# Performance work log

Hardware: AMD Instinct MI355X
Metric: run time of the kernel (lower is better)

The kernel has to match this reference:

```python
import jax, jax.numpy as jnp
import numpy as np

VOCAB = 50257
EMB = 256
HID = 512
BATCH = 32
SEQ = 512
PAD_ID = 0


def setup_inputs() -> dict:
    key = jax.random.key(0)
    k1, k2, k3, k4, k5, k6 = jax.random.split(key, 6)
    input_ids = jax.random.randint(k1, (BATCH, SEQ), 0, VOCAB, dtype=jnp.int32)
    attention_mask = jax.random.randint(k2, (BATCH, SEQ), 0, 2, dtype=jnp.int32)
    # learned params
    embed_table = jax.random.normal(k3, (VOCAB, EMB), dtype=jnp.float32) * 0.02
    Wx = jax.random.normal(k4, (EMB, HID), dtype=jnp.float32) / np.sqrt(EMB)
    Wh = jax.random.normal(k5, (HID, HID), dtype=jnp.float32) / np.sqrt(HID)
    b = jnp.zeros((HID,), dtype=jnp.float32)
    return {"input_ids": input_ids, "attention_mask": attention_mask,
            "embed_table": embed_table, "Wx": Wx, "Wh": Wh, "b": b}


def reference(input_ids, attention_mask, embed_table, Wx, Wh, b):
    # Embedding lookup: [B, S, E]
    emb = embed_table[input_ids]
    # time-major for scan: [S, B, E] and [S, B]
    xs = jnp.swapaxes(emb, 0, 1)
    ms = jnp.swapaxes(attention_mask, 0, 1)
    h0 = jnp.zeros((emb.shape[0], Wh.shape[0]), dtype=emb.dtype)

    def step(h, xm):
        x_t, m_t = xm  # [B, E], [B]
        h_new = jnp.tanh(x_t @ Wx + h @ Wh + b)  # Elman RNN cell
        h_next = jnp.where((m_t != PAD_ID)[:, None], h_new, h)
        return h_next, h_next

    final_h, all_h_tmajor = jax.lax.scan(step, h0, (xs, ms))
    all_h = jnp.swapaxes(all_h_tmajor, 0, 1)  # [B, S, H]
    return all_h, final_h
```

## Files before the change

kernel.cpp:

```cpp
#include <hip/hip_runtime.h>

#define VOCAB 50257
#define EMB 256
#define HID 512
#define BATCH 32
#define SEQ 512

typedef _Float16 h2 __attribute__((ext_vector_type(2)));

#if __has_builtin(__builtin_amdgcn_fdot2)
#define FDOT2(a, b, c) __builtin_amdgcn_fdot2((a), (b), (c), false)
#else
static __device__ __forceinline__ float FDOT2(h2 a, h2 b, float c) {
    return c + (float)a.x * (float)b.x + (float)a.y * (float)b.y;
}
#endif

static __device__ __forceinline__ h2 mk2(float a, float b) {
    h2 r; r.x = (_Float16)a; r.y = (_Float16)b; return r;
}

__global__ __launch_bounds__(256) void xprec_kernel(
    const int* __restrict__ ids, const float* __restrict__ emb,
    const float* __restrict__ Wx, const float* __restrict__ bias,
    float* __restrict__ allh)
{
    __shared__ float embL[16][EMB];
    const int tid  = threadIdx.x;
    const int tok0 = blockIdx.x * 16;

    {
        const int t    = tid >> 4;
        const int part = tid & 15;
        const int id   = ids[tok0 + t];
        const float4* src = (const float4*)(emb + (size_t)id * EMB + part * 16);
        float4* dst = (float4*)(&embL[t][part * 16]);
        dst[0] = src[0]; dst[1] = src[1]; dst[2] = src[2]; dst[3] = src[3];
    }
    __syncthreads();

    const int j0 = tid * 2;
    float2 acc[16];
    const float2 bv = *(const float2*)(bias + j0);
#pragma unroll
    for (int t = 0; t < 16; ++t) acc[t] = bv;

    for (int e = 0; e < EMB; e += 4) {
        const float2 w0 = *(const float2*)(Wx + (size_t)(e + 0) * HID + j0);
        const float2 w1 = *(const float2*)(Wx + (size_t)(e + 1) * HID + j0);
        const float2 w2 = *(const float2*)(Wx + (size_t)(e + 2) * HID + j0);
        const float2 w3 = *(const float2*)(Wx + (size_t)(e + 3) * HID + j0);
#pragma unroll
        for (int t = 0; t < 16; ++t) {
            const float4 ev = *(const float4*)(&embL[t][e]);
            acc[t].x += ev.x * w0.x + ev.y * w1.x + ev.z * w2.x + ev.w * w3.x;
            acc[t].y += ev.x * w0.y + ev.y * w1.y + ev.z * w2.y + ev.w * w3.y;
        }
    }

#pragma unroll
    for (int t = 0; t < 16; ++t) {
        *(float2*)(allh + (size_t)(tok0 + t) * HID + j0) = acc[t];
    }
}

__global__ __launch_bounds__(512, 2) void rnn_local_kernel(
    const int* __restrict__ mask, const float* __restrict__ Wh,
    float* __restrict__ allh, float* __restrict__ finalh)
{
    __shared__ h2    wlds[2][32][512];
    __shared__ float zp[8][8][64];
    __shared__ h2    h2L[256];
    __shared__ int   mlist[SEQ];
    __shared__ int   nmL;

    const int tid = threadIdx.x;
    const int b   = blockIdx.x;
    const int c   = tid & 63;
    const int p   = tid >> 6;

    int* maskL = (int*)zp;
    maskL[tid] = mask[b * SEQ + tid];
    __syncthreads();
    if (tid == 0) {
        int n = 0;
        for (int t = 0; t < SEQ; ++t) if (maskL[t]) mlist[n++] = t;
        nmL = n;
    }

    const float* wb = Wh + (size_t)(64 * p) * HID + c;
    h2 wv0[32], wv1[32], wv2[32], wv3[32], wv4[32], wv5[32];
#pragma unroll
    for (int i = 0; i < 32; ++i) {
        const float* r0 = wb + (size_t)(2 * i) * HID;
        const float* r1 = r0 + HID;
        wv0[i] = mk2(r0[0 * 64], r1[0 * 64]);
        wv1[i] = mk2(r0[1 * 64], r1[1 * 64]);
        wv2[i] = mk2(r0[2 * 64], r1[2 * 64]);
        wv3[i] = mk2(r0[3 * 64], r1[3 * 64]);
        wv4[i] = mk2(r0[4 * 64], r1[4 * 64]);
        wv5[i] = mk2(r0[5 * 64], r1[5 * 64]);
        wlds[0][i][tid] = mk2(r0[6 * 64], r1[6 * 64]);
        wlds[1][i][tid] = mk2(r0[7 * 64], r1[7 * 64]);
    }
    if (tid < 256) h2L[tid] = mk2(0.f, 0.f);

    __syncthreads();
    const int nm = nmL;

    float* arow = allh + (size_t)b * SEQ * HID;

    {
        const int end0 = nm ? mlist[0] : SEQ;
        for (int t = 0; t < end0; ++t) arow[(size_t)t * HID + tid] = 0.f;
    }

    float hreg  = 0.f;
    float xnext = 0.f;
    if (nm) xnext = arow[(size_t)mlist[0] * HID + tid];

    for (int i = 0; i < nm; ++i) {
        const int t    = mlist[i];
        const int tend = (i + 1 < nm) ? mlist[i + 1] : SEQ;
        const float x  = xnext;
        if (i + 1 < nm)
            xnext = arow[(size_t)mlist[i + 1] * HID + tid];

        float a0 = 0.f, a1 = 0.f, a2 = 0.f, a3 = 0.f;
        float a4 = 0.f, a5 = 0.f, a6 = 0.f, a7 = 0.f;
        const h2* hp = &h2L[32 * p];
#pragma unroll
        for (int i2 = 0; i2 < 32; ++i2) {
            const h2 hv = hp[i2];
            a0 = FDOT2(wv0[i2], hv, a0);
            a1 = FDOT2(wv1[i2], hv, a1);
            a2 = FDOT2(wv2[i2], hv, a2);
            a3 = FDOT2(wv3[i2], hv, a3);
            a4 = FDOT2(wv4[i2], hv, a4);
            a5 = FDOT2(wv5[i2], hv, a5);
            a6 = FDOT2(wlds[0][i2][tid], hv, a6);
            a7 = FDOT2(wlds[1][i2][tid], hv, a7);
        }
        zp[p][0][c] = a0; zp[p][1][c] = a1; zp[p][2][c] = a2; zp[p][3][c] = a3;
        zp[p][4][c] = a4; zp[p][5][c] = a5; zp[p][6][c] = a6; zp[p][7][c] = a7;
        __syncthreads();

        const float z = zp[0][p][c] + zp[1][p][c] + zp[2][p][c] + zp[3][p][c]
                      + zp[4][p][c] + zp[5][p][c] + zp[6][p][c] + zp[7][p][c];
        const float hn = tanhf(x + z);
        hreg = hn;
        ((_Float16*)h2L)[tid] = (_Float16)hn;
        for (int tt = t; tt < tend; ++tt)
            arow[(size_t)tt * HID + tid] = hreg;
        __syncthreads();
    }
    finalh[b * HID + tid] = hreg;
}

extern "C" void kernel_launch(void* const* d_in, const int* in_sizes, int n_in,
                              void* d_out, int out_size, void* d_ws, size_t ws_size,
                              hipStream_t stream) {
    const int*   ids  = (const int*)d_in[0];
    const int*   msk  = (const int*)d_in[1];
    const float* emb  = (const float*)d_in[2];
    const float* Wx   = (const float*)d_in[3];
    const float* Wh   = (const float*)d_in[4];
    const float* bias = (const float*)d_in[5];

    float* allh   = (float*)d_out;
    float* finalh = (float*)d_out + (size_t)BATCH * SEQ * HID;

    xprec_kernel<<<BATCH * SEQ / 16, 256, 0, stream>>>(ids, emb, Wx, bias, allh);
    rnn_local_kernel<<<BATCH, 512, 0, stream>>>(msk, Wh, allh, finalh);
}
```

Before: 669.8 us.

## Broadcast hidden state via readlane and vectorize LDS weights; enlarge input-projection tile

In the recurrent kernel, each wave consumes only the hidden units it produced itself. The fp16 hidden state is therefore packed with a lane shuffle and broadcast into scalar registers with readlane, which removes the LDS h buffer and its per-step reads. The LDS-resident weight columns are repacked as uint4 so that one wide load brings in four fp16 pairs. The input-projection kernel now processes 32 tokens per block instead of 16, reusing each Wx load across more tokens at the cost of more accumulator registers and fewer blocks.

```diff
diff --git a/kernel.cpp b/kernel.cpp
--- a/kernel.cpp
+++ b/kernel.cpp
@@ -7,6 +7,7 @@
 #define SEQ 512
 
 typedef _Float16 h2 __attribute__((ext_vector_type(2)));
+typedef unsigned int u32;
 
 #if __has_builtin(__builtin_amdgcn_fdot2)
 #define FDOT2(a, b, c) __builtin_amdgcn_fdot2((a), (b), (c), false)
@@ -19,31 +20,38 @@
 static __device__ __forceinline__ h2 mk2(float a, float b) {
     h2 r; r.x = (_Float16)a; r.y = (_Float16)b; return r;
 }
+static __device__ __forceinline__ u32 pk_rtn(float a, float b) {
+    return __builtin_bit_cast(u32, mk2(a, b));
+}
+static __device__ __forceinline__ h2 as_h2(u32 v) {
+    return __builtin_bit_cast(h2, v);
+}
 
 __global__ __launch_bounds__(256) void xprec_kernel(
     const int* __restrict__ ids, const float* __restrict__ emb,
     const float* __restrict__ Wx, const float* __restrict__ bias,
     float* __restrict__ allh)
 {
-    __shared__ float embL[16][EMB];
+    __shared__ float embL[32][EMB];
     const int tid  = threadIdx.x;
-    const int tok0 = blockIdx.x * 16;
+    const int tok0 = blockIdx.x * 32;
 
     {
-        const int t    = tid >> 4;
-        const int part = tid & 15;
+        const int t    = tid >> 3;
+        const int part = tid & 7;
         const int id   = ids[tok0 + t];
-        const float4* src = (const float4*)(emb + (size_t)id * EMB + part * 16);
-        float4* dst = (float4*)(&embL[t][part * 16]);
-        dst[0] = src[0]; dst[1] = src[1]; dst[2] = src[2]; dst[3] = src[3];
+        const float4* src = (const float4*)(emb + (size_t)id * EMB + part * 32);
+        float4* dst = (float4*)(&embL[t][part * 32]);
+#pragma unroll
+        for (int k = 0; k < 8; ++k) dst[k] = src[k];
     }
     __syncthreads();
 
     const int j0 = tid * 2;
-    float2 acc[16];
+    float2 acc[32];
     const float2 bv = *(const float2*)(bias + j0);
 #pragma unroll
-    for (int t = 0; t < 16; ++t) acc[t] = bv;
+    for (int t = 0; t < 32; ++t) acc[t] = bv;
 
     for (int e = 0; e < EMB; e += 4) {
         const float2 w0 = *(const float2*)(Wx + (size_t)(e + 0) * HID + j0);
@@ -51,7 +59,7 @@
         const float2 w2 = *(const float2*)(Wx + (size_t)(e + 2) * HID + j0);
         const float2 w3 = *(const float2*)(Wx + (size_t)(e + 3) * HID + j0);
 #pragma unroll
-        for (int t = 0; t < 16; ++t) {
+        for (int t = 0; t < 32; ++t) {
             const float4 ev = *(const float4*)(&embL[t][e]);
             acc[t].x += ev.x * w0.x + ev.y * w1.x + ev.z * w2.x + ev.w * w3.x;
             acc[t].y += ev.x * w0.y + ev.y * w1.y + ev.z * w2.y + ev.w * w3.y;
@@ -59,7 +67,7 @@
     }
 
 #pragma unroll
-    for (int t = 0; t < 16; ++t) {
+    for (int t = 0; t < 32; ++t) {
         *(float2*)(allh + (size_t)(tok0 + t) * HID + j0) = acc[t];
     }
 }
@@ -68,9 +76,8 @@
     const int* __restrict__ mask, const float* __restrict__ Wh,
     float* __restrict__ allh, float* __restrict__ finalh)
 {
-    __shared__ h2    wlds[2][32][512];
+    __shared__ uint4 wl[2][8][512];
     __shared__ float zp[8][8][64];
-    __shared__ h2    h2L[256];
     __shared__ int   mlist[SEQ];
     __shared__ int   nmL;
 
@@ -100,11 +107,21 @@
         wv3[i] = mk2(r0[3 * 64], r1[3 * 64]);
         wv4[i] = mk2(r0[4 * 64], r1[4 * 64]);
         wv5[i] = mk2(r0[5 * 64], r1[5 * 64]);
-        wlds[0][i][tid] = mk2(r0[6 * 64], r1[6 * 64]);
-        wlds[1][i][tid] = mk2(r0[7 * 64], r1[7 * 64]);
-    }
-    if (tid < 256) h2L[tid] = mk2(0.f, 0.f);
-
+    }
+#pragma unroll
+    for (int blk = 0; blk < 8; ++blk) {
+        uint4 v6, v7;
+        u32* v6p = (u32*)&v6; u32* v7p = (u32*)&v7;
+#pragma unroll
+        for (int e = 0; e < 4; ++e) {
+            const float* r0 = wb + (size_t)(blk * 8 + 2 * e) * HID;
+            const float* r1 = r0 + HID;
+            v6p[e] = pk_rtn(r0[6 * 64], r1[6 * 64]);
+            v7p[e] = pk_rtn(r0[7 * 64], r1[7 * 64]);
+        }
+        wl[0][blk][tid] = v6;
+        wl[1][blk][tid] = v7;
+    }
     __syncthreads();
     const int nm = nmL;
 
@@ -115,31 +132,42 @@
         for (int t = 0; t < end0; ++t) arow[(size_t)t * HID + tid] = 0.f;
     }
 
+    u32 hs[32];
+#pragma unroll
+    for (int i = 0; i < 32; ++i) hs[i] = 0u;
+
     float hreg  = 0.f;
     float xnext = 0.f;
     if (nm) xnext = arow[(size_t)mlist[0] * HID + tid];
 
-    for (int i = 0; i < nm; ++i) {
-        const int t    = mlist[i];
-        const int tend = (i + 1 < nm) ? mlist[i + 1] : SEQ;
+    for (int it = 0; it < nm; ++it) {
+        const int t    = mlist[it];
+        const int tend = (it + 1 < nm) ? mlist[it + 1] : SEQ;
         const float x  = xnext;
-        if (i + 1 < nm)
-            xnext = arow[(size_t)mlist[i + 1] * HID + tid];
+        if (it + 1 < nm)
+            xnext = arow[(size_t)mlist[it + 1] * HID + tid];
 
         float a0 = 0.f, a1 = 0.f, a2 = 0.f, a3 = 0.f;
         float a4 = 0.f, a5 = 0.f, a6 = 0.f, a7 = 0.f;
-        const h2* hp = &h2L[32 * p];
-#pragma unroll
-        for (int i2 = 0; i2 < 32; ++i2) {
-            const h2 hv = hp[i2];
-            a0 = FDOT2(wv0[i2], hv, a0);
-            a1 = FDOT2(wv1[i2], hv, a1);
-            a2 = FDOT2(wv2[i2], hv, a2);
-            a3 = FDOT2(wv3[i2], hv, a3);
-            a4 = FDOT2(wv4[i2], hv, a4);
-            a5 = FDOT2(wv5[i2], hv, a5);
-            a6 = FDOT2(wlds[0][i2][tid], hv, a6);
-            a7 = FDOT2(wlds[1][i2][tid], hv, a7);
+#pragma unroll
+        for (int blk = 0; blk < 8; ++blk) {
+            const uint4 w6 = wl[0][blk][tid];
+            const uint4 w7 = wl[1][blk][tid];
+            const u32* w6p = (const u32*)&w6;
+            const u32* w7p = (const u32*)&w7;
+#pragma unroll
+            for (int e = 0; e < 4; ++e) {
+                const int i = blk * 4 + e;
+                const h2 hv = as_h2(hs[i]);
+                a0 = FDOT2(wv0[i], hv, a0);
+                a1 = FDOT2(wv1[i], hv, a1);
+                a2 = FDOT2(wv2[i], hv, a2);
+                a3 = FDOT2(wv3[i], hv, a3);
+                a4 = FDOT2(wv4[i], hv, a4);
+                a5 = FDOT2(wv5[i], hv, a5);
+                a6 = FDOT2(as_h2(w6p[e]), hv, a6);
+                a7 = FDOT2(as_h2(w7p[e]), hv, a7);
+            }
         }
         zp[p][0][c] = a0; zp[p][1][c] = a1; zp[p][2][c] = a2; zp[p][3][c] = a3;
         zp[p][4][c] = a4; zp[p][5][c] = a5; zp[p][6][c] = a6; zp[p][7][c] = a7;
@@ -149,9 +177,15 @@
                       + zp[4][p][c] + zp[5][p][c] + zp[6][p][c] + zp[7][p][c];
         const float hn = tanhf(x + z);
         hreg = hn;
-        ((_Float16*)h2L)[tid] = (_Float16)hn;
         for (int tt = t; tt < tend; ++tt)
-            arow[(size_t)tt * HID + tid] = hreg;
+            arow[(size_t)tt * HID + tid] = hn;
+
+        const float hpartner = __shfl_xor(hn, 1);
+        const u32 pku = pk_rtn(hn, hpartner);
+#pragma unroll
+        for (int i = 0; i < 32; ++i)
+            hs[i] = (u32)__builtin_amdgcn_readlane((int)pku, 2 * i);
+
         __syncthreads();
     }
     finalh[b * HID + tid] = hreg;
@@ -170,6 +204,6 @@
     float* allh   = (float*)d_out;
     float* finalh = (float*)d_out + (size_t)BATCH * SEQ * HID;
 
-    xprec_kernel<<<BATCH * SEQ / 16, 256, 0, stream>>>(ids, emb, Wx, bias, allh);
+    xprec_kernel<<<BATCH * SEQ / 32, 256, 0, stream>>>(ids, emb, Wx, bias, allh);
     rnn_local_kernel<<<BATCH, 512, 0, stream>>>(msk, Wh, allh, finalh);
 }
```

Measured after the change: 694.0 us. +3.6%, slower.
